# Optimization experiments

Measured on AMD Instinct MI355X. Metric: run time of the kernel, lower is better.

The kernel has to match this reference:

```python
import jax, jax.numpy as jnp
import numpy as np

N_HEADS = 8
D_EMBED = 512
D_HEAD = D_EMBED // N_HEADS  # used only for the scale factor, as in the source


def setup_inputs() -> dict:
    key = jax.random.key(0)
    k1, k2, k3, k4, k5 = jax.random.split(key, 5)
    B, S, D = 4, 4096, D_EMBED
    s = 1.0 / np.sqrt(D)
    return {
        "x": jax.random.normal(k1, (B, S, D), dtype=jnp.float32),
        "w_in": jax.random.normal(k2, (3 * D, D), dtype=jnp.float32) * s,
        "b_in": jax.random.normal(k3, (3 * D,), dtype=jnp.float32) * 0.01,
        "w_out": jax.random.normal(k4, (D, D), dtype=jnp.float32) * s,
        "b_out": jax.random.normal(k5, (D,), dtype=jnp.float32) * 0.01,
    }


def reference(x, w_in, b_in, w_out, b_out):
    # in_proj: torch Linear y = x @ W.T + b ; chunk into q,k,v along last dim
    qkv = jnp.einsum("bsd,ed->bse", x, w_in) + b_in  # [B,S,3D]
    q, k, v = jnp.split(qkv, 3, axis=-1)  # each [B,S,D]
    # NOTE: source never splits into heads; attention over full d_embed,
    # but scaled by sqrt(d_head) = sqrt(d_embed / n_heads).
    scores = jnp.einsum("bqd,bkd->bqk", q, k) / np.sqrt(D_HEAD)  # [B,S,S]
    weight = jax.nn.softmax(scores, axis=-1)
    out = jnp.einsum("bqk,bkd->bqd", weight, v)  # [B,S,D]
    out = jnp.einsum("bsd,ed->bse", out, w_out) + b_out
    return out
```

## Files before the change

### kernel.cpp

```cpp
#include <hip/hip_runtime.h>

typedef __bf16 bf16x8 __attribute__((ext_vector_type(8)));
typedef float f32x4 __attribute__((ext_vector_type(4)));

#define MFMA16(a, b, c) __builtin_amdgcn_mfma_f32_16x16x32_bf16(a, b, c, 0, 0, 0)
#define LOG2E 1.44269504088896340736f

__device__ __forceinline__ unsigned short f2bf(float f) {
  union { float f; unsigned u; } v; v.f = f;
  return (unsigned short)((v.u + 0x7fffu + ((v.u >> 16) & 1u)) >> 16);
}
__device__ __forceinline__ bf16x8 ld_frag(const unsigned short* p) {
  return *(const bf16x8*)p;
}
__device__ __forceinline__ void gld_lds16(const unsigned short* g, unsigned short* l) {
  __builtin_amdgcn_global_load_lds(
      (const __attribute__((address_space(1))) unsigned int*)(const void*)g,
      (__attribute__((address_space(3))) unsigned int*)(void*)l, 16, 0, 0);
}

__global__ void cvt_f2bf(const float* __restrict__ in,
                         unsigned short* __restrict__ out, int n4) {
  int i = blockIdx.x * blockDim.x + threadIdx.x;
  if (i < n4) {
    float4 v = ((const float4*)in)[i];
    ushort4 o;
    o.x = f2bf(v.x); o.y = f2bf(v.y); o.z = f2bf(v.z); o.w = f2bf(v.w);
    ((ushort4*)out)[i] = o;
  }
}

__global__ void gemm_bt(const unsigned short* __restrict__ A,
                        const unsigned short* __restrict__ B,
                        const float* __restrict__ bias,
                        float* __restrict__ outf,
                        unsigned short* __restrict__ qbuf,
                        unsigned short* __restrict__ kbuf,
                        unsigned short* __restrict__ vtbuf,
                        int M, int N, int K, int mode) {
  __shared__ alignas(16) unsigned short As[128 * 32];
  __shared__ alignas(16) unsigned short Bs[128 * 32];
  const int n0 = blockIdx.x * 128, m0 = blockIdx.y * 128;
  const int tid = threadIdx.x;
  const int l = tid & 63, w = tid >> 6;
  const int quad = l >> 4, c = l & 15;
  const int wm = (w >> 1) * 64, wn = (w & 1) * 64;

  f32x4 acc[4][4] = {};
  const int kiters = K >> 5;
  for (int kt = 0; kt < kiters; ++kt) {
    __syncthreads();
    const int kk = kt * 32 + (l & 3) * 8;
    const int row = l >> 2;
#pragma unroll
    for (int i = 0; i < 2; ++i) {
      const int rbase = i * 64 + w * 16;
      gld_lds16(&A[(size_t)(m0 + rbase + row) * K + kk], &As[rbase * 32]);
      gld_lds16(&B[(size_t)(n0 + rbase + row) * K + kk], &Bs[rbase * 32]);
    }
    __syncthreads();
    bf16x8 af[4], bfr[4];
#pragma unroll
    for (int t = 0; t < 4; ++t) {
      af[t] = ld_frag(&As[(wm + t * 16 + c) * 32 + quad * 8]);
      bfr[t] = ld_frag(&Bs[(wn + t * 16 + c) * 32 + quad * 8]);
    }
#pragma unroll
    for (int mt = 0; mt < 4; ++mt)
#pragma unroll
      for (int nt = 0; nt < 4; ++nt)
        acc[mt][nt] = MFMA16(af[mt], bfr[nt], acc[mt][nt]);
  }

#pragma unroll
  for (int nt = 0; nt < 4; ++nt) {
    const int n = n0 + wn + nt * 16 + c;
    const float bsum = bias[n];
#pragma unroll
    for (int mt = 0; mt < 4; ++mt) {
      const int mbase = m0 + wm + mt * 16 + quad * 4;
      if (mode == 0) {
#pragma unroll
        for (int r = 0; r < 4; ++r)
          outf[(size_t)(mbase + r) * N + n] = acc[mt][nt][r] + bsum;
      } else if (n < 1024) {
        unsigned short* dst = (n < 512) ? qbuf : kbuf;
        const int nn = n & 511;
#pragma unroll
        for (int r = 0; r < 4; ++r)
          dst[(size_t)(mbase + r) * 512 + nn] = f2bf(acc[mt][nt][r] + bsum);
      } else {
        const int d = n - 1024;
        const int bb = mbase >> 12, s = mbase & 4095;
        const int cidx = (s >> 2) & 7;
        const int sp = (s & ~31) | (((((cidx & 3) << 1) | (cidx >> 2))) << 2);
        ushort4 pk;
        pk.x = f2bf(acc[mt][nt][0] + bsum);
        pk.y = f2bf(acc[mt][nt][1] + bsum);
        pk.z = f2bf(acc[mt][nt][2] + bsum);
        pk.w = f2bf(acc[mt][nt][3] + bsum);
        *(ushort4*)&vtbuf[((size_t)bb * 512 + d) * 4096 + sp] = pk;
      }
    }
  }
}

#define KROW 520

__global__ __launch_bounds__(256, 2) void attn_kernel(
    const unsigned short* __restrict__ Q, const unsigned short* __restrict__ Kb,
    const unsigned short* __restrict__ Vt, unsigned short* __restrict__ part0,
    unsigned short* __restrict__ part1, float2* __restrict__ mlbuf) {
  __shared__ alignas(16) unsigned short k_lds[32 * KROW];
  __shared__ alignas(16) unsigned short v_lds[512 * 32];

  const int bid = blockIdx.x;
  const int xcd = bid & 7;
  const int b = xcd >> 1;
  const int half = (bid >> 3) & 1;
  const int qt = (bid >> 4) | ((xcd & 1) << 5);
  const int s0 = qt * 64;
  const int kvbase = half * 2048;
  const int tid = threadIdx.x;
  const int l = tid & 63, w = tid >> 6;
  const int quad = l >> 4, c = l & 15;
  const size_t boff = (size_t)b * 4096 * 512;

  const unsigned short* Kbase = Kb + boff;
  const unsigned short* Vbase = Vt + (size_t)b * 512 * 4096;

  auto stage_k = [&](int kv0) {
#pragma unroll
    for (int i = 0; i < 8; ++i) {
      const int row = i * 4 + w;
      gld_lds16(&Kbase[(size_t)(kv0 + row) * 512 + l * 8], &k_lds[row * KROW]);
    }
  };
  auto stage_v = [&](int kv0) {
#pragma unroll
    for (int i = 0; i < 8; ++i) {
      const int dbase = (i * 4 + w) * 16;
      const int d = dbase + (l >> 2);
      const int jl = (l & 3) ^ ((d >> 1) & 3);
      gld_lds16(&Vbase[(size_t)d * 4096 + kv0 + jl * 8], &v_lds[dbase * 32]);
    }
  };

  stage_k(kvbase);
  stage_v(kvbase);

  bf16x8 qf[16];
  {
    const unsigned short* qrow = Q + boff + (size_t)(s0 + w * 16 + c) * 512;
#pragma unroll
    for (int ks = 0; ks < 16; ++ks) qf[ks] = ld_frag(&qrow[ks * 32 + quad * 8]);
  }

  f32x4 o[32] = {};
  float m_run = -1e30f, l_run = 0.f;

  const float C1 = 0.125f * LOG2E;
  const int jp8 = (quad ^ ((c >> 1) & 3)) * 8;

  for (int it = 0; it < 64; ++it) {
    asm volatile("s_waitcnt vmcnt(8)" ::: "memory");
    __builtin_amdgcn_sched_barrier(0);
    __builtin_amdgcn_s_barrier();
    __builtin_amdgcn_sched_barrier(0);

    f32x4 sa[2][2] = {};
    __builtin_amdgcn_s_setprio(1);
#pragma unroll
    for (int ks = 0; ks < 16; ++ks) {
      const unsigned short* kr = &k_lds[c * KROW + ks * 32 + quad * 8];
      bf16x8 kf0 = ld_frag(kr);
      bf16x8 kf1 = ld_frag(kr + 16 * KROW);
      sa[0][ks & 1] = MFMA16(kf0, qf[ks], sa[0][ks & 1]);
      sa[1][ks & 1] = MFMA16(kf1, qf[ks], sa[1][ks & 1]);
    }
    __builtin_amdgcn_s_setprio(0);
    const f32x4 s0v = sa[0][0] + sa[0][1];
    const f32x4 s1v = sa[1][0] + sa[1][1];

    asm volatile("s_waitcnt vmcnt(0) lgkmcnt(0)" ::: "memory");
    __builtin_amdgcn_sched_barrier(0);
    __builtin_amdgcn_s_barrier();
    __builtin_amdgcn_sched_barrier(0);

    if (it + 1 < 64) stage_k(kvbase + (it + 1) * 32);

    float m8 = fmaxf(fmaxf(fmaxf(s0v[0], s0v[1]), fmaxf(s0v[2], s0v[3])),
                     fmaxf(fmaxf(s1v[0], s1v[1]), fmaxf(s1v[2], s1v[3])));
    m8 = fmaxf(m8, __shfl_xor(m8, 16));
    m8 = fmaxf(m8, __shfl_xor(m8, 32));

    const bool need = __any(m8 - m_run > 8.0f);
    if (need) {
      const float mn = fmaxf(m_run, m8);
      const float alpha = exp2f((m_run - mn) * C1);
      m_run = mn;
      l_run *= alpha;
#pragma unroll
      for (int t = 0; t < 32; ++t) o[t] *= alpha;
    }

    float p0[4], p1[4], s8 = 0.f;
#pragma unroll
    for (int r = 0; r < 4; ++r) {
      p0[r] = exp2f((s0v[r] - m_run) * C1);
      p1[r] = exp2f((s1v[r] - m_run) * C1);
      s8 += p0[r] + p1[r];
    }
    s8 += __shfl_xor(s8, 16);
    s8 += __shfl_xor(s8, 32);
    l_run += s8;

    union { bf16x8 v; unsigned u[4]; } pfu;
    pfu.u[0] = (unsigned)f2bf(p0[0]) | ((unsigned)f2bf(p0[1]) << 16);
    pfu.u[1] = (unsigned)f2bf(p0[2]) | ((unsigned)f2bf(p0[3]) << 16);
    pfu.u[2] = (unsigned)f2bf(p1[0]) | ((unsigned)f2bf(p1[1]) << 16);
    pfu.u[3] = (unsigned)f2bf(p1[2]) | ((unsigned)f2bf(p1[3]) << 16);
    const bf16x8 pf = pfu.v;

    __builtin_amdgcn_s_setprio(1);
#pragma unroll
    for (int t = 0; t < 32; ++t) {
      const bf16x8 vf = ld_frag(&v_lds[(t * 16 + c) * 32 + jp8]);
      o[t] = MFMA16(vf, pf, o[t]);
    }
    __builtin_amdgcn_s_setprio(0);

    asm volatile("s_waitcnt lgkmcnt(0)" ::: "memory");
    __builtin_amdgcn_sched_barrier(0);
    __builtin_amdgcn_s_barrier();
    __builtin_amdgcn_sched_barrier(0);

    if (it + 1 < 64) stage_v(kvbase + (it + 1) * 32);
  }

  const float inv = 1.0f / l_run;
  unsigned short* part = half ? part1 : part0;
  unsigned short* orow = part + boff + (size_t)(s0 + w * 16 + c) * 512;
#pragma unroll
  for (int t = 0; t < 32; ++t) {
    ushort4 pk;
    pk.x = f2bf(o[t][0] * inv);
    pk.y = f2bf(o[t][1] * inv);
    pk.z = f2bf(o[t][2] * inv);
    pk.w = f2bf(o[t][3] * inv);
    *(ushort4*)&orow[t * 16 + quad * 4] = pk;
  }
  if (quad == 0) {
    float2 ml; ml.x = m_run; ml.y = l_run;
    mlbuf[(size_t)half * 16384 + b * 4096 + s0 + w * 16 + c] = ml;
  }
}

__global__ void merge_halves(const unsigned short* __restrict__ p1,
                             const float2* __restrict__ mlbuf,
                             unsigned short* __restrict__ p0out) {
  const int i = blockIdx.x * blockDim.x + threadIdx.x;
  const int row = i >> 6;
  const float2 a = mlbuf[row];
  const float2 bb = mlbuf[16384 + row];
  const float C1 = 0.125f * LOG2E;
  const float M = fmaxf(a.x, bb.x);
  float w0 = a.y * exp2f((a.x - M) * C1);
  float w1 = bb.y * exp2f((bb.x - M) * C1);
  const float inv = 1.0f / (w0 + w1);
  w0 *= inv; w1 *= inv;
  bf16x8 v0 = *(const bf16x8*)(p0out + (size_t)i * 8);
  bf16x8 v1 = *(const bf16x8*)(p1 + (size_t)i * 8);
  ushort4 o0, o1;
  o0.x = f2bf(w0 * (float)v0[0] + w1 * (float)v1[0]);
  o0.y = f2bf(w0 * (float)v0[1] + w1 * (float)v1[1]);
  o0.z = f2bf(w0 * (float)v0[2] + w1 * (float)v1[2]);
  o0.w = f2bf(w0 * (float)v0[3] + w1 * (float)v1[3]);
  o1.x = f2bf(w0 * (float)v0[4] + w1 * (float)v1[4]);
  o1.y = f2bf(w0 * (float)v0[5] + w1 * (float)v1[5]);
  o1.z = f2bf(w0 * (float)v0[6] + w1 * (float)v1[6]);
  o1.w = f2bf(w0 * (float)v0[7] + w1 * (float)v1[7]);
  *(ushort4*)(p0out + (size_t)i * 8) = o0;
  *(ushort4*)(p0out + (size_t)i * 8 + 4) = o1;
}

extern "C" void kernel_launch(void* const* d_in, const int* in_sizes, int n_in,
                              void* d_out, int out_size, void* d_ws, size_t ws_size,
                              hipStream_t stream) {
  const float* x = (const float*)d_in[0];
  const float* w_in = (const float*)d_in[1];
  const float* b_in = (const float*)d_in[2];
  const float* w_out = (const float*)d_in[3];
  const float* b_out = (const float*)d_in[4];
  float* out = (float*)d_out;

  const size_t MTOT = (size_t)4 * 4096 * 512;
  unsigned short* q = (unsigned short*)d_ws;
  unsigned short* k = q + MTOT;
  unsigned short* vt = k + MTOT;
  unsigned short* xbf = vt + MTOT;
  unsigned short* part1 = xbf + MTOT;
  unsigned short* w_in_bf = part1 + MTOT;
  unsigned short* w_out_bf = w_in_bf + 1536 * 512;
  float2* mlbuf = (float2*)(w_out_bf + 512 * 512);

  cvt_f2bf<<<dim3((int)(MTOT / 4 / 256)), 256, 0, stream>>>(x, xbf,
                                                            (int)(MTOT / 4));
  cvt_f2bf<<<dim3(768), 256, 0, stream>>>(w_in, w_in_bf, 1536 * 512 / 4);
  cvt_f2bf<<<dim3(256), 256, 0, stream>>>(w_out, w_out_bf, 512 * 512 / 4);

  gemm_bt<<<dim3(12, 128), 256, 0, stream>>>(xbf, w_in_bf, b_in, nullptr, q, k,
                                             vt, 16384, 1536, 512, 1);
  attn_kernel<<<dim3(512), 256, 0, stream>>>(q, k, vt, xbf, part1, mlbuf);
  merge_halves<<<dim3(4096), 256, 0, stream>>>(part1, mlbuf, xbf);
  gemm_bt<<<dim3(4, 128), 256, 0, stream>>>(xbf, w_out_bf, b_out, out, nullptr,
                                            nullptr, nullptr, 16384, 512, 512,
                                            0);
}
```

Before: 428.7 us.

## Double-buffer GEMM with BK=64 swizzled LDS and fuse split-K merge into out-proj

The bf16 GEMM now loads K-tiles of 64 into a two-stage LDS ring with an XOR swizzle. The load for the next tile is issued before computing on the current one, so there is one barrier per iteration instead of two. The separate merge_halves kernel is removed: the output-projection GEMM (mode 2) reads both attention partials and their max/sum stats and does the weighted merge while staging the A tile. This saves one launch and a full round trip of the merged activation through memory. The cost is more LDS per block, extra ALU work in the A staging path, and an A load that goes through registers instead of direct-to-LDS for the out-proj.

```diff
diff --git a/kernel.cpp b/kernel.cpp
--- a/kernel.cpp
+++ b/kernel.cpp
@@ -30,46 +30,80 @@
   }
 }
 
-__global__ void gemm_bt(const unsigned short* __restrict__ A,
-                        const unsigned short* __restrict__ B,
-                        const float* __restrict__ bias,
-                        float* __restrict__ outf,
-                        unsigned short* __restrict__ qbuf,
-                        unsigned short* __restrict__ kbuf,
-                        unsigned short* __restrict__ vtbuf,
-                        int M, int N, int K, int mode) {
-  __shared__ alignas(16) unsigned short As[128 * 32];
-  __shared__ alignas(16) unsigned short Bs[128 * 32];
+__global__ __launch_bounds__(256, 2) void gemm_bt(
+    const unsigned short* __restrict__ A, const unsigned short* __restrict__ B,
+    const float* __restrict__ bias, float* __restrict__ outf,
+    unsigned short* __restrict__ qbuf, unsigned short* __restrict__ kbuf,
+    unsigned short* __restrict__ vtbuf, int M, int N, int K, int mode) {
+  __shared__ alignas(16) unsigned short As[2 * 128 * 64];
+  __shared__ alignas(16) unsigned short Bs[2 * 128 * 64];
   const int n0 = blockIdx.x * 128, m0 = blockIdx.y * 128;
   const int tid = threadIdx.x;
   const int l = tid & 63, w = tid >> 6;
   const int quad = l >> 4, c = l & 15;
   const int wm = (w >> 1) * 64, wn = (w & 1) * 64;
+  const int srow = l >> 3;
+  const int gsw = (l & 7) ^ (srow & 7);
+  const float C1m = 0.125f * LOG2E;
+
+  const unsigned short* p1base = qbuf;
+  const float2* ml = (const float2*)kbuf;
+
+  auto stage = [&](int kt, int bsel) {
+    const int kk = kt * 64;
+    const int lb = bsel * 8192;
+#pragma unroll
+    for (int i = 0; i < 4; ++i) {
+      const int rb = i * 32 + w * 8;
+      gld_lds16(&B[(size_t)(n0 + rb + srow) * K + kk + gsw * 8],
+                &Bs[lb + rb * 64]);
+      if (mode != 2) {
+        gld_lds16(&A[(size_t)(m0 + rb + srow) * K + kk + gsw * 8],
+                  &As[lb + rb * 64]);
+      } else {
+        const int r = m0 + rb + srow;
+        const bf16x8 v0 = ld_frag(&A[(size_t)r * K + kk + gsw * 8]);
+        const bf16x8 v1 = ld_frag(&p1base[(size_t)r * K + kk + gsw * 8]);
+        const float2 ma = ml[r];
+        const float2 mb = ml[16384 + r];
+        const float Mx = fmaxf(ma.x, mb.x);
+        float w0 = ma.y * exp2f((ma.x - Mx) * C1m);
+        float w1 = mb.y * exp2f((mb.x - Mx) * C1m);
+        const float inv = 1.0f / (w0 + w1);
+        w0 *= inv; w1 *= inv;
+        union { bf16x8 v; ushort4 s4[2]; } pk;
+#pragma unroll
+        for (int e = 0; e < 8; ++e) {
+          const float mv = w0 * (float)v0[e] + w1 * (float)v1[e];
+          ((unsigned short*)&pk)[e] = f2bf(mv);
+        }
+        *(bf16x8*)&As[lb + (rb + srow) * 64 + (l & 7) * 8] = pk.v;
+      }
+    }
+  };
 
   f32x4 acc[4][4] = {};
-  const int kiters = K >> 5;
+  const int kiters = K >> 6;
+  stage(0, 0);
   for (int kt = 0; kt < kiters; ++kt) {
     __syncthreads();
-    const int kk = kt * 32 + (l & 3) * 8;
-    const int row = l >> 2;
-#pragma unroll
-    for (int i = 0; i < 2; ++i) {
-      const int rbase = i * 64 + w * 16;
-      gld_lds16(&A[(size_t)(m0 + rbase + row) * K + kk], &As[rbase * 32]);
-      gld_lds16(&B[(size_t)(n0 + rbase + row) * K + kk], &Bs[rbase * 32]);
-    }
-    __syncthreads();
-    bf16x8 af[4], bfr[4];
-#pragma unroll
-    for (int t = 0; t < 4; ++t) {
-      af[t] = ld_frag(&As[(wm + t * 16 + c) * 32 + quad * 8]);
-      bfr[t] = ld_frag(&Bs[(wn + t * 16 + c) * 32 + quad * 8]);
-    }
-#pragma unroll
-    for (int mt = 0; mt < 4; ++mt)
-#pragma unroll
-      for (int nt = 0; nt < 4; ++nt)
-        acc[mt][nt] = MFMA16(af[mt], bfr[nt], acc[mt][nt]);
+    if (kt + 1 < kiters) stage(kt + 1, (kt + 1) & 1);
+    const int lb = (kt & 1) * 8192;
+#pragma unroll
+    for (int ks = 0; ks < 2; ++ks) {
+      bf16x8 af[4], bfr[4];
+      const int gsel = ((ks * 4 + quad) ^ (c & 7)) * 8;
+#pragma unroll
+      for (int t = 0; t < 4; ++t) {
+        af[t] = ld_frag(&As[lb + (wm + t * 16 + c) * 64 + gsel]);
+        bfr[t] = ld_frag(&Bs[lb + (wn + t * 16 + c) * 64 + gsel]);
+      }
+#pragma unroll
+      for (int mt = 0; mt < 4; ++mt)
+#pragma unroll
+        for (int nt = 0; nt < 4; ++nt)
+          acc[mt][nt] = MFMA16(af[mt], bfr[nt], acc[mt][nt]);
+    }
   }
 
 #pragma unroll
@@ -79,7 +113,7 @@
 #pragma unroll
     for (int mt = 0; mt < 4; ++mt) {
       const int mbase = m0 + wm + mt * 16 + quad * 4;
-      if (mode == 0) {
+      if (mode != 1) {
 #pragma unroll
         for (int r = 0; r < 4; ++r)
           outf[(size_t)(mbase + r) * N + n] = acc[mt][nt][r] + bsum;
@@ -256,34 +290,6 @@
   }
 }
 
-__global__ void merge_halves(const unsigned short* __restrict__ p1,
-                             const float2* __restrict__ mlbuf,
-                             unsigned short* __restrict__ p0out) {
-  const int i = blockIdx.x * blockDim.x + threadIdx.x;
-  const int row = i >> 6;
-  const float2 a = mlbuf[row];
-  const float2 bb = mlbuf[16384 + row];
-  const float C1 = 0.125f * LOG2E;
-  const float M = fmaxf(a.x, bb.x);
-  float w0 = a.y * exp2f((a.x - M) * C1);
-  float w1 = bb.y * exp2f((bb.x - M) * C1);
-  const float inv = 1.0f / (w0 + w1);
-  w0 *= inv; w1 *= inv;
-  bf16x8 v0 = *(const bf16x8*)(p0out + (size_t)i * 8);
-  bf16x8 v1 = *(const bf16x8*)(p1 + (size_t)i * 8);
-  ushort4 o0, o1;
-  o0.x = f2bf(w0 * (float)v0[0] + w1 * (float)v1[0]);
-  o0.y = f2bf(w0 * (float)v0[1] + w1 * (float)v1[1]);
-  o0.z = f2bf(w0 * (float)v0[2] + w1 * (float)v1[2]);
-  o0.w = f2bf(w0 * (float)v0[3] + w1 * (float)v1[3]);
-  o1.x = f2bf(w0 * (float)v0[4] + w1 * (float)v1[4]);
-  o1.y = f2bf(w0 * (float)v0[5] + w1 * (float)v1[5]);
-  o1.z = f2bf(w0 * (float)v0[6] + w1 * (float)v1[6]);
-  o1.w = f2bf(w0 * (float)v0[7] + w1 * (float)v1[7]);
-  *(ushort4*)(p0out + (size_t)i * 8) = o0;
-  *(ushort4*)(p0out + (size_t)i * 8 + 4) = o1;
-}
-
 extern "C" void kernel_launch(void* const* d_in, const int* in_sizes, int n_in,
                               void* d_out, int out_size, void* d_ws, size_t ws_size,
                               hipStream_t stream) {
@@ -312,8 +318,7 @@
   gemm_bt<<<dim3(12, 128), 256, 0, stream>>>(xbf, w_in_bf, b_in, nullptr, q, k,
                                              vt, 16384, 1536, 512, 1);
   attn_kernel<<<dim3(512), 256, 0, stream>>>(q, k, vt, xbf, part1, mlbuf);
-  merge_halves<<<dim3(4096), 256, 0, stream>>>(part1, mlbuf, xbf);
-  gemm_bt<<<dim3(4, 128), 256, 0, stream>>>(xbf, w_out_bf, b_out, out, nullptr,
-                                            nullptr, nullptr, 16384, 512, 512,
-                                            0);
-}
+  gemm_bt<<<dim3(4, 128), 256, 0, stream>>>(xbf, w_out_bf, b_out, out, part1,
+                                            (unsigned short*)mlbuf, nullptr,
+                                            16384, 512, 512, 2);
+}
```

Result: no change. 431.2 us (+0.6%).
